# Kernel tuning notes

Hardware: AMD Instinct MI355X
Metric: run time of the kernel (lower is better)

The kernel has to match this reference:

```python
import jax, jax.numpy as jnp
import numpy as np

N_AGENTS = 32
BROADCAST = 1
HIDDEN = 64
R, T = 16, 512
D_IN = (N_AGENTS - 1) * (3 + BROADCAST)  # 124
D_OUT = 2 + BROADCAST  # 3


def setup_inputs() -> dict:
    key = jax.random.key(0)
    ks = jax.random.split(key, 8)
    runs = jax.random.normal(ks[0], (R, T, N_AGENTS, N_AGENTS - 1, 3), jnp.float32)
    # init_comm(): uniform(1, 2) of shape (broadcast, N) per run
    comm_init = jax.random.uniform(ks[1], (R, BROADCAST, N_AGENTS), jnp.float32, 1.0, 2.0)
    scale = 0.05  # keep tanh out of saturation
    w1 = jax.random.normal(ks[2], (HIDDEN, D_IN), jnp.float32) * scale
    b1 = jax.random.normal(ks[3], (HIDDEN,), jnp.float32) * scale
    w2 = jax.random.normal(ks[4], (HIDDEN, HIDDEN), jnp.float32) * scale
    b2 = jax.random.normal(ks[5], (HIDDEN,), jnp.float32) * scale
    w3 = jax.random.normal(ks[6], (D_OUT, HIDDEN), jnp.float32) * scale
    b3 = jax.random.normal(ks[7], (D_OUT,), jnp.float32) * scale
    return {"runs": runs, "comm_init": comm_init, "w1": w1, "b1": b1,
            "w2": w2, "b2": b2, "w3": w3, "b3": b3}


def reference(runs, comm_init, w1, b1, w2, b2, w3, b3):
    # runs: [R, T, N, N-1, 3]; comm_init: [R, broadcast, N]
    Rr, Tt, Nn = runs.shape[0], runs.shape[1], runs.shape[2]
    # skip_diag_strided: row i = all agent indices except i, in order
    n_closest = jnp.asarray(
        np.array([[j for j in range(Nn) if j != i] for i in range(Nn)]), jnp.int32)
    agent_ids = jnp.arange(Nn, dtype=jnp.int32)

    def snet(x):  # eval mode: dropout disabled
        h = jnp.tanh(x @ w1.T + b1)
        h = jnp.tanh(h @ w2.T + b2)
        return h @ w3.T + b3  # [2 + broadcast]

    def agent_step(comm, inp):
        xs_i, idx_i, i = inp  # xs_i: [N-1, 3], idx_i: [N-1]
        rel = comm[:, idx_i]  # [broadcast, N-1] gather of neighbor comm
        x = jnp.concatenate([xs_i.reshape(-1), rel.reshape(-1)])  # [D_IN]
        out = snet(x)
        # comm update is detached in torch (output[2:].detach().numpy())
        comm = comm.at[:, i].set(jax.lax.stop_gradient(out[2:]))
        return comm, out[:2]

    def t_step(comm, xs_t):  # sequential scatter-update across agents
        comm, ctrl = jax.lax.scan(agent_step, comm, (xs_t, n_closest, agent_ids))
        return comm, ctrl  # ctrl: [N, 2]

    def run_fn(run, c0):
        _, controls = jax.lax.scan(t_step, c0, run)  # [T, N, 2]
        return controls

    return jax.vmap(run_fn)(runs, comm_init)  # [R, T, N, 2]
```

## Files before the change

kernel.cpp:

```cpp
#include <hip/hip_runtime.h>


#define R_RUNS 16
#define T_STEPS 512
#define NA 32
#define HID 64
#define XS 93
#define DIN 124
#define STEPS_PER_RUN (T_STEPS * NA)
#define RTI_TOT (R_RUNS * STEPS_PER_RUN)

#define PRE1_OFF 65536
#define WS_NEEDED ((size_t)PRE1_OFF + (size_t)RTI_TOT * HID * 4 + 4096)

typedef _Float16 half2_t __attribute__((ext_vector_type(2)));
typedef unsigned int uint2v __attribute__((ext_vector_type(2)));

#if defined(__has_builtin)
#if __has_builtin(__builtin_amdgcn_permlane16_swap) && __has_builtin(__builtin_amdgcn_permlane32_swap)
#define HAVE_PLSWAP 1
#endif
#endif
#ifndef HAVE_PLSWAP
#define HAVE_PLSWAP 0
#endif

#if defined(__has_builtin)
#if __has_builtin(__builtin_amdgcn_exp2f)
#define EXPFN(x) __builtin_amdgcn_exp2f(x)
#define SC 2.8853900817779268f
#define HAVE_EXP2 1
#endif
#endif
#ifndef HAVE_EXP2
#define EXPFN(x) __expf(x)
#define SC 2.0f
#define HAVE_EXP2 0
#endif

__device__ __forceinline__ float fast_tanh(float x) {
  float e = __expf(2.f * x);
  return fmaf(-2.f, __builtin_amdgcn_rcpf(e + 1.f), 1.f);
}

__device__ __forceinline__ float dot2h(half2_t a, half2_t b, float c) {
#if __has_builtin(__builtin_amdgcn_fdot2)
  return __builtin_amdgcn_fdot2(a, b, c, false);
#else
  return fmaf((float)a.x, (float)b.x, fmaf((float)a.y, (float)b.y, c));
#endif
}

__device__ __forceinline__ half2_t bch(unsigned u) {
  return __builtin_bit_cast(half2_t, u);
}

#define DPP_ADD(x, ctrl, rmask) \
  (x) += __int_as_float(__builtin_amdgcn_update_dpp(0, __float_as_int(x), (ctrl), (rmask), 0xf, true))

__device__ __forceinline__ float wave64_sum_bcast(float x) {
  DPP_ADD(x, 0x111, 0xf);
  DPP_ADD(x, 0x112, 0xf);
  DPP_ADD(x, 0x114, 0xf);
  DPP_ADD(x, 0x118, 0xf);
  DPP_ADD(x, 0x142, 0xa);
  DPP_ADD(x, 0x143, 0xc);
  return __int_as_float(__builtin_amdgcn_readlane(__float_as_int(x), 63));
}

__device__ __forceinline__ float wave64_sum_all(float x) {
  DPP_ADD(x, 0xB1, 0xf);
  DPP_ADD(x, 0x4E, 0xf);
  DPP_ADD(x, 0x141, 0xf);
  DPP_ADD(x, 0x140, 0xf);
#if HAVE_PLSWAP
  uint2v p = __builtin_amdgcn_permlane16_swap(__float_as_uint(x), __float_as_uint(x), false, false);
  x = __uint_as_float(p[0]) + __uint_as_float(p[1]);
  p = __builtin_amdgcn_permlane32_swap(__float_as_uint(x), __float_as_uint(x), false, false);
  x = __uint_as_float(p[0]) + __uint_as_float(p[1]);
  return x;
#else
  DPP_ADD(x, 0x142, 0xa);
  DPP_ADD(x, 0x143, 0xc);
  return __int_as_float(__builtin_amdgcn_readlane(__float_as_int(x), 63));
#endif
}

__global__ void transpose_w1(const float* __restrict__ w1, float* __restrict__ w1T4) {
  int idx = blockIdx.x * blockDim.x + threadIdx.x;
  if (idx < 24 * HID * 4) {
    int c = idx & 3, h = (idx >> 2) & 63, kk = idx >> 8;
    int k = 4 * kk + c;
    w1T4[idx] = (k < XS) ? w1[h * DIN + k] : 0.f;
  }
}

#define PRE1_BATCH 4
__global__ __launch_bounds__(256) void pre1_kernel(
    const float* __restrict__ runs, const float* __restrict__ w1T4,
    const float* __restrict__ b1, float* __restrict__ pre1) {
  const int wid = (blockIdx.x * 256 + threadIdx.x) >> 6;
  const int lane = threadIdx.x & 63;
  const int rti0 = wid * PRE1_BATCH;
  const float4* wv = (const float4*)w1T4;
  float4 w[24];
#pragma unroll
  for (int kk = 0; kk < 24; ++kk) w[kk] = wv[kk * 64 + lane];
  const float b1s = b1[lane];
#pragma unroll
  for (int u = 0; u < PRE1_BATCH; ++u) {
    const float* xs = runs + (size_t)(rti0 + u) * XS;
    float a0 = b1s, a1 = 0.f, a2 = 0.f, a3 = 0.f;
#pragma unroll
    for (int kk = 0; kk < 23; ++kk) {
      a0 = fmaf(xs[4 * kk + 0], w[kk].x, a0);
      a1 = fmaf(xs[4 * kk + 1], w[kk].y, a1);
      a2 = fmaf(xs[4 * kk + 2], w[kk].z, a2);
      a3 = fmaf(xs[4 * kk + 3], w[kk].w, a3);
    }
    a0 = fmaf(xs[92], w[23].x, a0);
    pre1[(size_t)(rti0 + u) * HID + lane] = SC * ((a0 + a1) + (a2 + a3));
  }
}

__global__ __launch_bounds__(256) void out_kernel(
    const float* __restrict__ h2, const float* __restrict__ w3,
    const float* __restrict__ b3, float* __restrict__ out) {
  const int rti = blockIdx.x * 256 + threadIdx.x;
  const float4* hv4 = (const float4*)(h2 + (size_t)rti * HID);
  const float4* w0v = (const float4*)w3;
  const float4* w1v = (const float4*)(w3 + HID);
  float p00 = 0.f, p01 = 0.f, p02 = 0.f, p03 = 0.f;
  float p10 = 0.f, p11 = 0.f, p12 = 0.f, p13 = 0.f;
#pragma unroll
  for (int k = 0; k < 16; ++k) {
    float4 hv = hv4[k];
    float4 w0 = w0v[k];
    float4 w1r = w1v[k];
    p00 = fmaf(w0.x, hv.x, p00);  p01 = fmaf(w0.y, hv.y, p01);
    p02 = fmaf(w0.z, hv.z, p02);  p03 = fmaf(w0.w, hv.w, p03);
    p10 = fmaf(w1r.x, hv.x, p10); p11 = fmaf(w1r.y, hv.y, p11);
    p12 = fmaf(w1r.z, hv.z, p12); p13 = fmaf(w1r.w, hv.w, p13);
  }
  float o0 = ((p00 + p01) + (p02 + p03)) + b3[0];
  float o1 = ((p10 + p11) + (p12 + p13)) + b3[1];
  *(float2*)(out + (size_t)rti * 2) = make_float2(o0, o1);
}

__global__ __launch_bounds__(64, 1) void seq_kernel(
    const float* __restrict__ w1, const float* __restrict__ w2,
    const float* __restrict__ b2, const float* __restrict__ w3,
    const float* __restrict__ b3, const float* __restrict__ comm_init,
    float* pre1h2) {
  const int h = threadIdx.x;
  const int r = blockIdx.x;

  __shared__ __align__(16) float commL[NA];
  __shared__ __align__(16) _Float16 h1s16[HID];
  __shared__ __align__(16) float pbuf[2][2048 + 64];

  float A2r[33], B2r[33];
#pragma unroll
  for (int j = 0; j < 31; ++j) A2r[j] = SC * w1[h * DIN + 93 + j];
  A2r[31] = 0.f;
  A2r[32] = 0.f;
  B2r[0] = 0.f;
#pragma unroll
  for (int j = 1; j < 32; ++j) B2r[j] = SC * w1[h * DIN + 92 + j];
  B2r[32] = 0.f;

  const float* wOwn = w2 + h * HID;
  float rsum = 0.f;
#pragma unroll
  for (int k = 0; k < HID; ++k) rsum += wOwn[k];

#if HAVE_PLSWAP
  const int hi = h >> 5;
  const float4* wA = (const float4*)(w2 + h * HID + hi * 32);
  const float4* wB = (const float4*)(w2 + (h ^ 32) * HID + hi * 32);
  const float4 A0 = wA[0], A1 = wA[1], A2v = wA[2], A3 = wA[3];
  const float4 A4 = wA[4], A5 = wA[5], A6 = wA[6], A7 = wA[7];
  const float4 B0 = wB[0], B1 = wB[1], B2v = wB[2], B3 = wB[3];
  const float4 B4 = wB[4], B5 = wB[5], B6 = wB[6], B7 = wB[7];
#define PK2N(n, f4) \
  const half2_t n##a = {(_Float16)(-2.f * SC * (f4).x), (_Float16)(-2.f * SC * (f4).y)}; \
  const half2_t n##b = {(_Float16)(-2.f * SC * (f4).z), (_Float16)(-2.f * SC * (f4).w)}
  PK2N(pa0, A0); PK2N(pa1, A1); PK2N(pa2, A2v); PK2N(pa3, A3);
  PK2N(pa4, A4); PK2N(pa5, A5); PK2N(pa6, A6);  PK2N(pa7, A7);
  PK2N(pb0, B0); PK2N(pb1, B1); PK2N(pb2, B2v); PK2N(pb3, B3);
  PK2N(pb4, B4); PK2N(pb5, B5); PK2N(pb6, B6);  PK2N(pb7, B7);
#undef PK2N
#else
  const float4* w2v = (const float4*)(w2 + h * HID);
  const float4 r0 = w2v[0],  r1q = w2v[1], r2q = w2v[2],  r3q = w2v[3];
  const float4 r4 = w2v[4],  r5 = w2v[5],  r6 = w2v[6],  r7 = w2v[7];
  const float4 r8 = w2v[8],  r9 = w2v[9],  r10 = w2v[10], r11 = w2v[11];
  const float4 r12 = w2v[12], r13 = w2v[13], r14 = w2v[14], r15 = w2v[15];
#define PK2N(n, f4) \
  const half2_t n##a = {(_Float16)(-2.f * SC * (f4).x), (_Float16)(-2.f * SC * (f4).y)}; \
  const half2_t n##b = {(_Float16)(-2.f * SC * (f4).z), (_Float16)(-2.f * SC * (f4).w)}
  PK2N(q0, r0);  PK2N(q1, r1q); PK2N(q2, r2q); PK2N(q3, r3q);
  PK2N(q4, r4);  PK2N(q5, r5);  PK2N(q6, r6);  PK2N(q7, r7);
  PK2N(q8, r8);  PK2N(q9, r9);  PK2N(q10, r10); PK2N(q11, r11);
  PK2N(q12, r12); PK2N(q13, r13); PK2N(q14, r14); PK2N(q15, r15);
#undef PK2N
#endif

  const float base2 = SC * b2[h] + SC * rsum;
  const float w32h = w3[2 * HID + h];
  const float w32n2 = -2.f * w32h;
  const float b32 = b3[2];

  float commR = (h < NA) ? comm_init[r * NA + h] : 0.f;
  if (h < NA) commL[h] = commR;

  float* prow = pre1h2 + (size_t)r * STEPS_PER_RUN * HID;

  {
    const float4* s0 = (const float4*)prow;
    const float4* s1 = (const float4*)(prow + 2048);
    float4* d0 = (float4*)&pbuf[0][0];
    float4* d1 = (float4*)&pbuf[1][0];
#pragma unroll
    for (int j = 0; j < 8; ++j) d0[j * 64 + h] = s0[j * 64 + h];
#pragma unroll
    for (int j = 0; j < 8; ++j) d1[j * 64 + h] = s1[j * 64 + h];
  }

  for (int t = 0; t < T_STEPS; ++t) {
    float* pb = pbuf[t & 1];
    int tk = (t + 2 <= T_STEPS - 1) ? t + 2 : T_STEPS - 1;
    const float4* gsrc = (const float4*)(prow + (size_t)tk * 2048);
    float4 g0 = gsrc[0 * 64 + h], g1 = gsrc[1 * 64 + h];
    float4 g2 = gsrc[2 * 64 + h], g3 = gsrc[3 * 64 + h];
    float4 g4 = gsrc[4 * 64 + h], g5 = gsrc[5 * 64 + h];
    float4 g6 = gsrc[6 * 64 + h], g7 = gsrc[7 * 64 + h];

    const float4* cv4 = (const float4*)commL;
    float f0 = 0.f, f1 = 0.f, f2 = 0.f, f3 = 0.f;
#pragma unroll
    for (int q = 0; q < 8; ++q) {
      float4 c = cv4[q];
      f0 = fmaf(B2r[4 * q + 0], c.x, f0);
      f1 = fmaf(B2r[4 * q + 1], c.y, f1);
      f2 = fmaf(B2r[4 * q + 2], c.z, f2);
      f3 = fmaf(B2r[4 * q + 3], c.w, f3);
    }
    const float FB2 = (f0 + f1) + (f2 + f3);
    const float c0s = commR;
    float Q2 = 0.f, S2 = 0.f;
    float E = pb[h] + FB2;
    float* h2t = prow + (size_t)t * 2048;

#pragma unroll
    for (int i = 0; i < NA; ++i) {
      float pf2_n = pb[(i + 1) * 64 + h];
      float old_n = __int_as_float(__builtin_amdgcn_readlane(__float_as_int(c0s), i + 1));
      float e1 = EXPFN(E);
      float r1v = __builtin_amdgcn_rcpf(e1 + 1.f);
      h1s16[h] = (_Float16)r1v;
      float S2n = fmaf(B2r[i + 1], old_n, S2);
      float Qb2 = fmaf(A2r[i], b32, Q2);
      float H = pf2_n + (FB2 - S2n) + Qb2;
      float y2;
#if HAVE_PLSWAP
      const uint4* hv = (const uint4*)h1s16;
      uint4 X0 = hv[hi * 4 + 0], X1 = hv[hi * 4 + 1];
      uint4 X2 = hv[hi * 4 + 2], X3 = hv[hi * 4 + 3];
      float a0 = base2, a1 = 0.f, a2 = 0.f, a3 = 0.f;
#define DOTP(Xq, e, o) \
      a0 = dot2h(pa##e##a, bch(Xq.x), a0); a2 = dot2h(pb##e##a, bch(Xq.x), a2); \
      a1 = dot2h(pa##e##b, bch(Xq.y), a1); a3 = dot2h(pb##e##b, bch(Xq.y), a3); \
      a0 = dot2h(pa##o##a, bch(Xq.z), a0); a2 = dot2h(pb##o##a, bch(Xq.z), a2); \
      a1 = dot2h(pa##o##b, bch(Xq.w), a1); a3 = dot2h(pb##o##b, bch(Xq.w), a3)
      DOTP(X0, 0, 1); DOTP(X1, 2, 3); DOTP(X2, 4, 5); DOTP(X3, 6, 7);
#undef DOTP
      float pA = a0 + a1;
      float pBo = a2 + a3;
      uint2v sw = __builtin_amdgcn_permlane32_swap(
          __float_as_uint(pBo), __float_as_uint(pBo), false, false);
      float pB = hi ? __uint_as_float(sw[0]) : __uint_as_float(sw[1]);
      y2 = pA + pB;
#else
      const uint4* hv = (const uint4*)h1s16;
      uint4 X0 = hv[0], X1 = hv[1], X2 = hv[2], X3 = hv[3];
      uint4 X4 = hv[4], X5 = hv[5], X6 = hv[6], X7 = hv[7];
      float a0 = base2, a1 = 0.f, a2 = 0.f, a3 = 0.f;
#define DOTB(Xq, qe, qo) \
      a0 = dot2h(qe##a, bch(Xq.x), a0); a1 = dot2h(qe##b, bch(Xq.y), a1); \
      a2 = dot2h(qo##a, bch(Xq.z), a2); a3 = dot2h(qo##b, bch(Xq.w), a3)
      DOTB(X0, q0, q1);   DOTB(X1, q2, q3);
      DOTB(X2, q4, q5);   DOTB(X3, q6, q7);
      DOTB(X4, q8, q9);   DOTB(X5, q10, q11);
      DOTB(X6, q12, q13); DOTB(X7, q14, q15);
#undef DOTB
      y2 = (a0 + a1) + (a2 + a3);
#endif
      float e2 = EXPFN(y2);
      float r2v = __builtin_amdgcn_rcpf(e2 + 1.f);
      float xr = fmaf(w32n2, r2v, w32h);
      float csum = wave64_sum_all(xr);
      float h2v = fmaf(-2.f, r2v, 1.f);
      h2t[i * 64 + h] = h2v;
      float c_new = csum + b32;
      commR = (h == i) ? c_new : commR;
      E = fmaf(A2r[i], csum, H);
      Q2 = fmaf(A2r[i], csum, Qb2);
      S2 = S2n;
    }
    if (h < NA) commL[h] = commR;
    float4* pd = (float4*)pb;
    pd[0 * 64 + h] = g0; pd[1 * 64 + h] = g1;
    pd[2 * 64 + h] = g2; pd[3 * 64 + h] = g3;
    pd[4 * 64 + h] = g4; pd[5 * 64 + h] = g5;
    pd[6 * 64 + h] = g6; pd[7 * 64 + h] = g7;
  }
}

__global__ __launch_bounds__(64, 1) void seq_fused(
    const float* __restrict__ runs, const float* __restrict__ comm_init,
    const float* __restrict__ w1, const float* __restrict__ b1,
    const float* __restrict__ w2, const float* __restrict__ b2,
    const float* __restrict__ w3, const float* __restrict__ b3,
    float* __restrict__ out) {
  const int r = blockIdx.x;
  const int h = threadIdx.x;
  const int hb = h * 33;

  __shared__ float Asl[HID * 33];
  __shared__ float Bsl[HID * 33];
  __shared__ float commL[NA];
  __shared__ __align__(16) float h1s[HID];
  __shared__ float w1xs[XS * HID];
  __shared__ __align__(16) float xsl[96];

  for (int j = 0; j < 31; ++j) Asl[hb + j] = w1[h * DIN + 93 + j];
  Asl[hb + 31] = 0.f;
  Bsl[hb] = 0.f;
  for (int j = 1; j < 32; ++j) Bsl[hb + j] = w1[h * DIN + 92 + j];
  for (int k = 0; k < XS; ++k) w1xs[k * HID + h] = w1[h * DIN + k];

  float w2r[HID];
#pragma unroll
  for (int k = 0; k < HID; ++k) w2r[k] = w2[h * HID + k];
  const float b1h = b1[h];
  const float b2h = b2[h];
  const float w30h = w3[h], w31h = w3[HID + h], w32h = w3[2 * HID + h];
  const float b30 = b3[0], b31 = b3[1], b32 = b3[2];
  if (h < NA) commL[h] = comm_init[r * NA + h];

  const float* xbase = runs + (size_t)r * STEPS_PER_RUN * XS;
  float xa = xbase[h];
  float xb = (h < XS - 64) ? xbase[64 + h] : 0.f;
  float* outp = out + (size_t)r * STEPS_PER_RUN * 2;
  __syncthreads();

  int s = 0;
  for (int t = 0; t < T_STEPS; ++t) {
    float FB = 0.f;
#pragma unroll
    for (int j = 0; j < NA; ++j) FB = fmaf(Bsl[hb + j], commL[j], FB);
    float Q = 0.f, S = 0.f;
    for (int i = 0; i < NA; ++i, ++s) {
      int sn = s + 1; if (sn > STEPS_PER_RUN - 1) sn = STEPS_PER_RUN - 1;
      const float* xn = xbase + (size_t)sn * XS;
      xsl[h] = xa;
      if (h < XS - 64) xsl[64 + h] = xb;
      __syncthreads();
      float xa_n = xn[h];
      float xb_n = (h < XS - 64) ? xn[64 + h] : 0.f;
      float a0 = b1h, a1 = 0.f, a2 = 0.f;
#pragma unroll 4
      for (int k = 0; k < 31; ++k) {
        a0 = fmaf(xsl[3 * k],     w1xs[(3 * k) * HID + h],     a0);
        a1 = fmaf(xsl[3 * k + 1], w1xs[(3 * k + 1) * HID + h], a1);
        a2 = fmaf(xsl[3 * k + 2], w1xs[(3 * k + 2) * HID + h], a2);
      }
      float old_i = commL[i];
      S = fmaf(Bsl[hb + i], old_i, S);
      float h1 = fast_tanh(((a0 + a1) + a2) + FB + Q - S);
      h1s[h] = h1;
      __syncthreads();
      float c0 = b2h, c1 = 0.f, c2 = 0.f, c3 = 0.f;
      const float4* hv4 = (const float4*)h1s;
#pragma unroll
      for (int k4 = 0; k4 < 16; ++k4) {
        float4 hv = hv4[k4];
        c0 = fmaf(w2r[4 * k4 + 0], hv.x, c0);
        c1 = fmaf(w2r[4 * k4 + 1], hv.y, c1);
        c2 = fmaf(w2r[4 * k4 + 2], hv.z, c2);
        c3 = fmaf(w2r[4 * k4 + 3], hv.w, c3);
      }
      float h2 = fast_tanh((c0 + c1) + (c2 + c3));
      float o0 = wave64_sum_bcast(w30h * h2) + b30;
      float o1 = wave64_sum_bcast(w31h * h2) + b31;
      float c_new = wave64_sum_bcast(w32h * h2) + b32;
      if (h == 0) *(float2*)(outp + (size_t)s * 2) = make_float2(o0, o1);
      Q = fmaf(Asl[hb + i], c_new, Q);
      if (h == i) commL[h] = c_new;
      __syncthreads();
      xa = xa_n; xb = xb_n;
    }
  }
}

extern "C" void kernel_launch(void* const* d_in, const int* in_sizes, int n_in,
                              void* d_out, int out_size, void* d_ws, size_t ws_size,
                              hipStream_t stream) {
  const float* runs = (const float*)d_in[0];
  const float* comm_init = (const float*)d_in[1];
  const float* w1 = (const float*)d_in[2];
  const float* b1 = (const float*)d_in[3];
  const float* w2 = (const float*)d_in[4];
  const float* b2 = (const float*)d_in[5];
  const float* w3 = (const float*)d_in[6];
  const float* b3 = (const float*)d_in[7];
  float* out = (float*)d_out;

  if (ws_size >= WS_NEEDED) {
    float* w1T4 = (float*)d_ws;
    float* pre1 = (float*)((char*)d_ws + PRE1_OFF);
    hipLaunchKernelGGL(transpose_w1, dim3((24 * HID * 4 + 255) / 256), dim3(256), 0, stream,
                       w1, w1T4);
    hipLaunchKernelGGL(pre1_kernel, dim3(RTI_TOT / (PRE1_BATCH * 4)), dim3(256), 0, stream,
                       runs, w1T4, b1, pre1);
    hipLaunchKernelGGL(seq_kernel, dim3(R_RUNS), dim3(64), 0, stream,
                       w1, w2, b2, w3, b3, comm_init, pre1);
    hipLaunchKernelGGL(out_kernel, dim3(RTI_TOT / 256), dim3(256), 0, stream,
                       pre1, w3, b3, out);
  } else {
    hipLaunchKernelGGL(seq_fused, dim3(R_RUNS), dim3(64), 0, stream,
                       runs, comm_init, w1, b1, w2, b2, w3, b3, out);
  }
}
```

Before: 3.837 ms.

## Interleave two independent runs per wavefront to hide serial latency

The sequential kernel now processes two runs per 64-thread block, interleaving the front half of one run's agent step with the back half of the other so their dependency chains overlap. The dot product, exp and cross-lane reduction latencies of one run are meant to be covered by independent work from the other. Block count halves to 8, so fewer CUs are used, and register and LDS pressure grow with the duplicated state.

Measured after the change: 6.873 ms. 79.1% more time.

```diff
diff --git a/kernel.cpp b/kernel.cpp
--- a/kernel.cpp
+++ b/kernel.cpp
@@ -153,11 +153,14 @@
     const float* __restrict__ b3, const float* __restrict__ comm_init,
     float* pre1h2) {
   const int h = threadIdx.x;
-  const int r = blockIdx.x;
-
-  __shared__ __align__(16) float commL[NA];
-  __shared__ __align__(16) _Float16 h1s16[HID];
-  __shared__ __align__(16) float pbuf[2][2048 + 64];
+  const int rA = blockIdx.x * 2;
+  const int rB = rA + 1;
+
+  __shared__ __align__(16) float commLA[NA];
+  __shared__ __align__(16) float commLB[NA];
+  __shared__ __align__(16) _Float16 h1sA[HID];
+  __shared__ __align__(16) _Float16 h1sB[HID];
+  __shared__ __align__(16) float pbuf[2][2][2048 + 64];
 
   float A2r[33], B2r[33];
 #pragma unroll
@@ -176,6 +179,7 @@
 
 #if HAVE_PLSWAP
   const int hi = h >> 5;
+  const int hi4 = hi * 4;
   const float4* wA = (const float4*)(w2 + h * HID + hi * 32);
   const float4* wB = (const float4*)(w2 + (h ^ 32) * HID + hi * 32);
   const float4 A0 = wA[0], A1 = wA[1], A2v = wA[2], A3 = wA[3];
@@ -190,6 +194,21 @@
   PK2N(pb0, B0); PK2N(pb1, B1); PK2N(pb2, B2v); PK2N(pb3, B3);
   PK2N(pb4, B4); PK2N(pb5, B5); PK2N(pb6, B6);  PK2N(pb7, B7);
 #undef PK2N
+#define DOTP(Xq, e, o) \
+      a0 = dot2h(pa##e##a, bch(Xq.x), a0); a2 = dot2h(pb##e##a, bch(Xq.x), a2); \
+      a1 = dot2h(pa##e##b, bch(Xq.y), a1); a3 = dot2h(pb##e##b, bch(Xq.y), a3); \
+      a0 = dot2h(pa##o##a, bch(Xq.z), a0); a2 = dot2h(pb##o##a, bch(Xq.z), a2); \
+      a1 = dot2h(pa##o##b, bch(Xq.w), a1); a3 = dot2h(pb##o##b, bch(Xq.w), a3)
+#define DOT_Y2(bufp, Y2OUT) { \
+      const uint4* hv_ = (const uint4*)(bufp); \
+      uint4 X0 = hv_[hi4 + 0], X1 = hv_[hi4 + 1]; \
+      uint4 X2 = hv_[hi4 + 2], X3 = hv_[hi4 + 3]; \
+      float a0 = base2, a1 = 0.f, a2 = 0.f, a3 = 0.f; \
+      DOTP(X0, 0, 1); DOTP(X1, 2, 3); DOTP(X2, 4, 5); DOTP(X3, 6, 7); \
+      float pA_ = a0 + a1, pBo_ = a2 + a3; \
+      uint2v sw_ = __builtin_amdgcn_permlane32_swap( \
+          __float_as_uint(pBo_), __float_as_uint(pBo_), false, false); \
+      Y2OUT = pA_ + (hi ? __uint_as_float(sw_[0]) : __uint_as_float(sw_[1])); }
 #else
   const float4* w2v = (const float4*)(w2 + h * HID);
   const float4 r0 = w2v[0],  r1q = w2v[1], r2q = w2v[2],  r3q = w2v[3];
@@ -204,6 +223,19 @@
   PK2N(q8, r8);  PK2N(q9, r9);  PK2N(q10, r10); PK2N(q11, r11);
   PK2N(q12, r12); PK2N(q13, r13); PK2N(q14, r14); PK2N(q15, r15);
 #undef PK2N
+#define DOTB(Xq, qe, qo) \
+      a0 = dot2h(qe##a, bch(Xq.x), a0); a1 = dot2h(qe##b, bch(Xq.y), a1); \
+      a2 = dot2h(qo##a, bch(Xq.z), a2); a3 = dot2h(qo##b, bch(Xq.w), a3)
+#define DOT_Y2(bufp, Y2OUT) { \
+      const uint4* hv_ = (const uint4*)(bufp); \
+      uint4 X0 = hv_[0], X1 = hv_[1], X2 = hv_[2], X3 = hv_[3]; \
+      uint4 X4 = hv_[4], X5 = hv_[5], X6 = hv_[6], X7 = hv_[7]; \
+      float a0 = base2, a1 = 0.f, a2 = 0.f, a3 = 0.f; \
+      DOTB(X0, q0, q1);   DOTB(X1, q2, q3); \
+      DOTB(X2, q4, q5);   DOTB(X3, q6, q7); \
+      DOTB(X4, q8, q9);   DOTB(X5, q10, q11); \
+      DOTB(X6, q12, q13); DOTB(X7, q14, q15); \
+      Y2OUT = (a0 + a1) + (a2 + a3); }
 #endif
 
   const float base2 = SC * b2[h] + SC * rsum;
@@ -211,109 +243,130 @@
   const float w32n2 = -2.f * w32h;
   const float b32 = b3[2];
 
-  float commR = (h < NA) ? comm_init[r * NA + h] : 0.f;
-  if (h < NA) commL[h] = commR;
-
-  float* prow = pre1h2 + (size_t)r * STEPS_PER_RUN * HID;
+  float commRA = (h < NA) ? comm_init[rA * NA + h] : 0.f;
+  float commRB = (h < NA) ? comm_init[rB * NA + h] : 0.f;
+  if (h < NA) commLA[h] = commRA;
+  if (h < NA) commLB[h] = commRB;
+
+  float* prowA = pre1h2 + (size_t)rA * STEPS_PER_RUN * HID;
+  float* prowB = pre1h2 + (size_t)rB * STEPS_PER_RUN * HID;
 
   {
-    const float4* s0 = (const float4*)prow;
-    const float4* s1 = (const float4*)(prow + 2048);
-    float4* d0 = (float4*)&pbuf[0][0];
-    float4* d1 = (float4*)&pbuf[1][0];
-#pragma unroll
-    for (int j = 0; j < 8; ++j) d0[j * 64 + h] = s0[j * 64 + h];
-#pragma unroll
-    for (int j = 0; j < 8; ++j) d1[j * 64 + h] = s1[j * 64 + h];
+#pragma unroll
+    for (int run = 0; run < 2; ++run) {
+      const float* pr = run ? prowB : prowA;
+      const float4* s0 = (const float4*)pr;
+      const float4* s1 = (const float4*)(pr + 2048);
+      float4* d0 = (float4*)&pbuf[run][0][0];
+      float4* d1 = (float4*)&pbuf[run][1][0];
+#pragma unroll
+      for (int j = 0; j < 8; ++j) d0[j * 64 + h] = s0[j * 64 + h];
+#pragma unroll
+      for (int j = 0; j < 8; ++j) d1[j * 64 + h] = s1[j * 64 + h];
+    }
   }
 
   for (int t = 0; t < T_STEPS; ++t) {
-    float* pb = pbuf[t & 1];
+    float* pbA = pbuf[0][t & 1];
+    float* pbB = pbuf[1][t & 1];
     int tk = (t + 2 <= T_STEPS - 1) ? t + 2 : T_STEPS - 1;
-    const float4* gsrc = (const float4*)(prow + (size_t)tk * 2048);
-    float4 g0 = gsrc[0 * 64 + h], g1 = gsrc[1 * 64 + h];
-    float4 g2 = gsrc[2 * 64 + h], g3 = gsrc[3 * 64 + h];
-    float4 g4 = gsrc[4 * 64 + h], g5 = gsrc[5 * 64 + h];
-    float4 g6 = gsrc[6 * 64 + h], g7 = gsrc[7 * 64 + h];
-
-    const float4* cv4 = (const float4*)commL;
-    float f0 = 0.f, f1 = 0.f, f2 = 0.f, f3 = 0.f;
-#pragma unroll
-    for (int q = 0; q < 8; ++q) {
-      float4 c = cv4[q];
-      f0 = fmaf(B2r[4 * q + 0], c.x, f0);
-      f1 = fmaf(B2r[4 * q + 1], c.y, f1);
-      f2 = fmaf(B2r[4 * q + 2], c.z, f2);
-      f3 = fmaf(B2r[4 * q + 3], c.w, f3);
+    const float4* gsA = (const float4*)(prowA + (size_t)tk * 2048);
+    const float4* gsB = (const float4*)(prowB + (size_t)tk * 2048);
+    float4 gA0 = gsA[0 * 64 + h], gA1 = gsA[1 * 64 + h];
+    float4 gA2 = gsA[2 * 64 + h], gA3 = gsA[3 * 64 + h];
+    float4 gA4 = gsA[4 * 64 + h], gA5 = gsA[5 * 64 + h];
+    float4 gA6 = gsA[6 * 64 + h], gA7 = gsA[7 * 64 + h];
+    float4 gB0 = gsB[0 * 64 + h], gB1 = gsB[1 * 64 + h];
+    float4 gB2 = gsB[2 * 64 + h], gB3 = gsB[3 * 64 + h];
+    float4 gB4 = gsB[4 * 64 + h], gB5 = gsB[5 * 64 + h];
+    float4 gB6 = gsB[6 * 64 + h], gB7 = gsB[7 * 64 + h];
+
+    float FB2A, FB2B;
+    {
+      const float4* cv4 = (const float4*)commLA;
+      float f0 = 0.f, f1 = 0.f, f2 = 0.f, f3 = 0.f;
+#pragma unroll
+      for (int q = 0; q < 8; ++q) {
+        float4 c = cv4[q];
+        f0 = fmaf(B2r[4 * q + 0], c.x, f0);
+        f1 = fmaf(B2r[4 * q + 1], c.y, f1);
+        f2 = fmaf(B2r[4 * q + 2], c.z, f2);
+        f3 = fmaf(B2r[4 * q + 3], c.w, f3);
+      }
+      FB2A = (f0 + f1) + (f2 + f3);
+      const float4* dv4 = (const float4*)commLB;
+      float e0 = 0.f, e1 = 0.f, e2 = 0.f, e3 = 0.f;
+#pragma unroll
+      for (int q = 0; q < 8; ++q) {
+        float4 c = dv4[q];
+        e0 = fmaf(B2r[4 * q + 0], c.x, e0);
+        e1 = fmaf(B2r[4 * q + 1], c.y, e1);
+        e2 = fmaf(B2r[4 * q + 2], c.z, e2);
+        e3 = fmaf(B2r[4 * q + 3], c.w, e3);
+      }
+      FB2B = (e0 + e1) + (e2 + e3);
     }
-    const float FB2 = (f0 + f1) + (f2 + f3);
-    const float c0s = commR;
-    float Q2 = 0.f, S2 = 0.f;
-    float E = pb[h] + FB2;
-    float* h2t = prow + (size_t)t * 2048;
-
-#pragma unroll
-    for (int i = 0; i < NA; ++i) {
-      float pf2_n = pb[(i + 1) * 64 + h];
-      float old_n = __int_as_float(__builtin_amdgcn_readlane(__float_as_int(c0s), i + 1));
-      float e1 = EXPFN(E);
-      float r1v = __builtin_amdgcn_rcpf(e1 + 1.f);
-      h1s16[h] = (_Float16)r1v;
-      float S2n = fmaf(B2r[i + 1], old_n, S2);
-      float Qb2 = fmaf(A2r[i], b32, Q2);
-      float H = pf2_n + (FB2 - S2n) + Qb2;
-      float y2;
-#if HAVE_PLSWAP
-      const uint4* hv = (const uint4*)h1s16;
-      uint4 X0 = hv[hi * 4 + 0], X1 = hv[hi * 4 + 1];
-      uint4 X2 = hv[hi * 4 + 2], X3 = hv[hi * 4 + 3];
-      float a0 = base2, a1 = 0.f, a2 = 0.f, a3 = 0.f;
-#define DOTP(Xq, e, o) \
-      a0 = dot2h(pa##e##a, bch(Xq.x), a0); a2 = dot2h(pb##e##a, bch(Xq.x), a2); \
-      a1 = dot2h(pa##e##b, bch(Xq.y), a1); a3 = dot2h(pb##e##b, bch(Xq.y), a3); \
-      a0 = dot2h(pa##o##a, bch(Xq.z), a0); a2 = dot2h(pb##o##a, bch(Xq.z), a2); \
-      a1 = dot2h(pa##o##b, bch(Xq.w), a1); a3 = dot2h(pb##o##b, bch(Xq.w), a3)
-      DOTP(X0, 0, 1); DOTP(X1, 2, 3); DOTP(X2, 4, 5); DOTP(X3, 6, 7);
-#undef DOTP
-      float pA = a0 + a1;
-      float pBo = a2 + a3;
-      uint2v sw = __builtin_amdgcn_permlane32_swap(
-          __float_as_uint(pBo), __float_as_uint(pBo), false, false);
-      float pB = hi ? __uint_as_float(sw[0]) : __uint_as_float(sw[1]);
-      y2 = pA + pB;
-#else
-      const uint4* hv = (const uint4*)h1s16;
-      uint4 X0 = hv[0], X1 = hv[1], X2 = hv[2], X3 = hv[3];
-      uint4 X4 = hv[4], X5 = hv[5], X6 = hv[6], X7 = hv[7];
-      float a0 = base2, a1 = 0.f, a2 = 0.f, a3 = 0.f;
-#define DOTB(Xq, qe, qo) \
-      a0 = dot2h(qe##a, bch(Xq.x), a0); a1 = dot2h(qe##b, bch(Xq.y), a1); \
-      a2 = dot2h(qo##a, bch(Xq.z), a2); a3 = dot2h(qo##b, bch(Xq.w), a3)
-      DOTB(X0, q0, q1);   DOTB(X1, q2, q3);
-      DOTB(X2, q4, q5);   DOTB(X3, q6, q7);
-      DOTB(X4, q8, q9);   DOTB(X5, q10, q11);
-      DOTB(X6, q12, q13); DOTB(X7, q14, q15);
-#undef DOTB
-      y2 = (a0 + a1) + (a2 + a3);
-#endif
-      float e2 = EXPFN(y2);
-      float r2v = __builtin_amdgcn_rcpf(e2 + 1.f);
-      float xr = fmaf(w32n2, r2v, w32h);
-      float csum = wave64_sum_all(xr);
-      float h2v = fmaf(-2.f, r2v, 1.f);
-      h2t[i * 64 + h] = h2v;
-      float c_new = csum + b32;
-      commR = (h == i) ? c_new : commR;
-      E = fmaf(A2r[i], csum, H);
-      Q2 = fmaf(A2r[i], csum, Qb2);
-      S2 = S2n;
+    const float c0sA = commRA;
+    const float c0sB = commRB;
+    float Q2A = 0.f, S2A = 0.f, Q2B = 0.f, S2B = 0.f;
+    float EA = pbA[h] + FB2A;
+    float EB = pbB[h] + FB2B;
+    float* h2tA = prowA + (size_t)t * 2048;
+    float* h2tB = prowB + (size_t)t * 2048;
+    float HA, QbA, S2nA;
+    float HB, QbB, S2nB;
+
+#define FRONT(P, i) { \
+      float e1_ = EXPFN(E##P); \
+      float r1_ = __builtin_amdgcn_rcpf(e1_ + 1.f); \
+      h1s##P[h] = (_Float16)r1_; \
+      float pfn_ = pb##P[((i) + 1) * 64 + h]; \
+      float old_ = __int_as_float(__builtin_amdgcn_readlane( \
+          __float_as_int(c0s##P), (i) + 1)); \
+      S2n##P = fmaf(B2r[(i) + 1], old_, S2##P); \
+      Qb##P = fmaf(A2r[(i)], b32, Q2##P); \
+      H##P = pfn_ + (FB2##P - S2n##P) + Qb##P; }
+
+#define BACK(P, i) { \
+      float y2_; \
+      DOT_Y2(h1s##P, y2_); \
+      float e2_ = EXPFN(y2_); \
+      float r2_ = __builtin_amdgcn_rcpf(e2_ + 1.f); \
+      float xr_ = fmaf(w32n2, r2_, w32h); \
+      float csum_ = wave64_sum_all(xr_); \
+      float h2v_ = fmaf(-2.f, r2_, 1.f); \
+      h2t##P[(i) * 64 + h] = h2v_; \
+      commR##P = (h == (i)) ? csum_ + b32 : commR##P; \
+      E##P = fmaf(A2r[(i)], csum_, H##P); \
+      Q2##P = fmaf(A2r[(i)], csum_, Qb##P); \
+      S2##P = S2n##P; }
+
+    FRONT(A, 0);
+    FRONT(B, 0);
+    BACK(A, 0);
+#pragma unroll
+    for (int i = 1; i < NA; ++i) {
+      FRONT(A, i);
+      BACK(B, i - 1);
+      FRONT(B, i);
+      BACK(A, i);
     }
-    if (h < NA) commL[h] = commR;
-    float4* pd = (float4*)pb;
-    pd[0 * 64 + h] = g0; pd[1 * 64 + h] = g1;
-    pd[2 * 64 + h] = g2; pd[3 * 64 + h] = g3;
-    pd[4 * 64 + h] = g4; pd[5 * 64 + h] = g5;
-    pd[6 * 64 + h] = g6; pd[7 * 64 + h] = g7;
+    BACK(B, NA - 1);
+#undef FRONT
+#undef BACK
+
+    if (h < NA) commLA[h] = commRA;
+    if (h < NA) commLB[h] = commRB;
+    float4* pdA = (float4*)pbA;
+    pdA[0 * 64 + h] = gA0; pdA[1 * 64 + h] = gA1;
+    pdA[2 * 64 + h] = gA2; pdA[3 * 64 + h] = gA3;
+    pdA[4 * 64 + h] = gA4; pdA[5 * 64 + h] = gA5;
+    pdA[6 * 64 + h] = gA6; pdA[7 * 64 + h] = gA7;
+    float4* pdB = (float4*)pbB;
+    pdB[0 * 64 + h] = gB0; pdB[1 * 64 + h] = gB1;
+    pdB[2 * 64 + h] = gB2; pdB[3 * 64 + h] = gB3;
+    pdB[4 * 64 + h] = gB4; pdB[5 * 64 + h] = gB5;
+    pdB[6 * 64 + h] = gB6; pdB[7 * 64 + h] = gB7;
   }
 }
 
@@ -424,7 +477,7 @@
                        w1, w1T4);
     hipLaunchKernelGGL(pre1_kernel, dim3(RTI_TOT / (PRE1_BATCH * 4)), dim3(256), 0, stream,
                        runs, w1T4, b1, pre1);
-    hipLaunchKernelGGL(seq_kernel, dim3(R_RUNS), dim3(64), 0, stream,
+    hipLaunchKernelGGL(seq_kernel, dim3(R_RUNS / 2), dim3(64), 0, stream,
                        w1, w2, b2, w3, b3, comm_init, pre1);
     hipLaunchKernelGGL(out_kernel, dim3(RTI_TOT / 256), dim3(256), 0, stream,
                        pre1, w3, b3, out);
```
